# Kernel optimization log

Measured on AMD Instinct MI355X. Metric: run time of the kernel, lower is better.

Reference implementation:

```python
import jax, jax.numpy as jnp
import numpy as np

B, S, D = 32, 2048, 1024
E, K = 64, 8
N_TAGS = 128


def setup_inputs() -> dict:
    key = jax.random.key(0)
    k1, k2, k3, k4, k5, k6 = jax.random.split(key, 6)
    hidden_states = jax.random.normal(k1, (B, S, D), dtype=jnp.float32)
    subw_indices = jax.random.randint(k2, (B, E, K), 0, S, dtype=jnp.int32)
    subw_counts = jax.random.randint(k3, (B, E), 1, K + 1, dtype=jnp.int32)
    num_entities = jax.random.randint(k4, (B,), 1, E + 1, dtype=jnp.int32)
    fc_w = jax.random.normal(k5, (N_TAGS, D), dtype=jnp.float32) * (1.0 / np.sqrt(D))
    fc_b = jax.random.normal(k6, (N_TAGS,), dtype=jnp.float32) * 0.01
    return {
        "hidden_states": hidden_states,
        "subw_indices": subw_indices,
        "subw_counts": subw_counts,
        "num_entities": num_entities,
        "fc_w": fc_w,
        "fc_b": fc_b,
    }


def reference(hidden_states, subw_indices, subw_counts, num_entities, fc_w, fc_b):
    # Gather subword embeddings: [B, E, K, D]
    flat_idx = subw_indices.reshape(B, E * K)                      # [B, E*K]
    gathered = jnp.take_along_axis(
        hidden_states, flat_idx[:, :, None], axis=1
    ).reshape(B, E, K, D)
    # Mask padded subword slots and mean-pool per entity
    subw_mask = (jnp.arange(K)[None, None, :] < subw_counts[:, :, None])  # [B,E,K]
    subw_mask = subw_mask.astype(hidden_states.dtype)
    ent_emb = jnp.einsum("bekd,bek->bed", gathered, subw_mask)
    ent_emb = ent_emb / subw_counts[:, :, None].astype(hidden_states.dtype)
    # Zero-pad entities past num_entities (original pads with zero_emb)
    ent_mask = (jnp.arange(E)[None, :] < num_entities[:, None])    # [B,E]
    ent_emb = ent_emb * ent_mask[:, :, None].astype(hidden_states.dtype)
    # fc applied to all positions (padded rows yield the bias, as in original)
    logits = jnp.einsum("bed,td->bet", ent_emb, fc_w) + fc_b
    return logits
```

## Files before the change

kernel.cpp:

```cpp
#include <hip/hip_runtime.h>

#define BB 32
#define SS 2048
#define DD 1024
#define EE 64
#define KK 8
#define TT 128
#define MM (BB * EE)

#define MT 8
#define KC 128
#define ASTR 1032
#define WSTR 136

typedef __attribute__((ext_vector_type(8))) short short8;
typedef __attribute__((ext_vector_type(4))) float f32x4;

__device__ __forceinline__ unsigned short f2bf(float f) {
    union { float f; unsigned int u; } v; v.f = f;
    unsigned int u = v.u + 0x7FFFu + ((v.u >> 16) & 1u);
    return (unsigned short)(u >> 16);
}

__global__ __launch_bounds__(256) void te_fused_kernel(
    const float* __restrict__ hs,
    const int*   __restrict__ subw_idx,
    const int*   __restrict__ subw_cnt,
    const int*   __restrict__ num_ent,
    const float* __restrict__ fc_w,
    const float* __restrict__ fc_b,
    float* __restrict__ out)
{
    __shared__ unsigned short As[MT][ASTR];
    __shared__ unsigned short Ws[TT][WSTR];

    const int mt   = blockIdx.x;
    const int t    = threadIdx.x;
    const int wid  = t >> 6;
    const int lane = t & 63;

    {
        const int r  = t >> 5;
        const int c  = t & 31;
        const int be = mt * MT + r;
        const int b  = be >> 6;
        const int e  = be & 63;
        const int cnt = subw_cnt[be];
        const int ne  = num_ent[b];
        const float scale = (e < ne) ? (1.0f / (float)cnt) : 0.0f;
        const int* idxp = subw_idx + (size_t)be * KK;

        float4 acc4[8];
        #pragma unroll
        for (int j = 0; j < 8; ++j) acc4[j] = make_float4(0.f, 0.f, 0.f, 0.f);

        for (int k = 0; k < cnt; ++k) {
            const int s = idxp[k];
            const float4* row = (const float4*)(hs + ((size_t)b * SS + s) * DD);
            #pragma unroll
            for (int j = 0; j < 8; ++j) {
                float4 v = row[j * 32 + c];
                acc4[j].x += v.x; acc4[j].y += v.y;
                acc4[j].z += v.z; acc4[j].w += v.w;
            }
        }
        #pragma unroll
        for (int j = 0; j < 8; ++j) {
            ushort4 o;
            o.x = f2bf(acc4[j].x * scale); o.y = f2bf(acc4[j].y * scale);
            o.z = f2bf(acc4[j].z * scale); o.w = f2bf(acc4[j].w * scale);
            *(ushort4*)&As[r][(j * 32 + c) * 4] = o;
        }
    }

    const int nbase = wid * 32;
    const int lm  = lane & 15;
    const int lq  = (lane >> 4) * 8;
    const int lmA = lm & 7;

    f32x4 acc0 = {0.f,0.f,0.f,0.f}, acc1 = {0.f,0.f,0.f,0.f};

    const int n = t >> 1;
    const int h = (t & 1) * 64;

    for (int kc = 0; kc < DD / KC; ++kc) {
        __syncthreads();
        {
            const float4* wrow = (const float4*)(fc_w + (size_t)n * DD + kc * KC + h);
            #pragma unroll
            for (int j = 0; j < 16; ++j) {
                float4 v = wrow[j];
                ushort4 o;
                o.x = f2bf(v.x); o.y = f2bf(v.y);
                o.z = f2bf(v.z); o.w = f2bf(v.w);
                *(ushort4*)&Ws[n][h + j * 4] = o;
            }
        }
        __syncthreads();

        #pragma unroll
        for (int kstep = 0; kstep < KC / 32; ++kstep) {
            const int ko = kstep * 32 + lq;
            short8 a  = *(const short8*)&As[lmA][kc * KC + ko];
            short8 b0 = *(const short8*)&Ws[nbase +  0 + lm][ko];
            short8 b1 = *(const short8*)&Ws[nbase + 16 + lm][ko];
            acc0 = __builtin_amdgcn_mfma_f32_16x16x32_bf16(a, b0, acc0, 0, 0, 0);
            acc1 = __builtin_amdgcn_mfma_f32_16x16x32_bf16(a, b1, acc1, 0, 0, 0);
        }
    }

    if (lane < 32) {
        const int mrow = mt * MT + (lane >> 4) * 4;
        const int c0 = nbase + lm;
        const float b0v = fc_b[c0];
        const float b1v = fc_b[c0 + 16];
        #pragma unroll
        for (int r = 0; r < 4; ++r) {
            float* o = out + (size_t)(mrow + r) * TT + c0;
            o[0]  = acc0[r] + b0v;
            o[16] = acc1[r] + b1v;
        }
    }
}

extern "C" void kernel_launch(void* const* d_in, const int* in_sizes, int n_in,
                              void* d_out, int out_size, void* d_ws, size_t ws_size,
                              hipStream_t stream) {
    const float* hs       = (const float*)d_in[0];
    const int*   subw_idx = (const int*)  d_in[1];
    const int*   subw_cnt = (const int*)  d_in[2];
    const int*   num_ent  = (const int*)  d_in[3];
    const float* fc_w     = (const float*)d_in[4];
    const float* fc_b     = (const float*)d_in[5];
    float*       out      = (float*)d_out;

    te_fused_kernel<<<MM / MT, 256, 0, stream>>>(
        hs, subw_idx, subw_cnt, num_ent, fc_w, fc_b, out);
}
```

Measured before the change: 327.5 us.

## Split fused pool+GEMM into separate pooling and bf16 GEMM kernels

Replaces the single fused kernel with two launches. The first pools the gathered subword rows (one block per entity), writes bf16 entity embeddings to workspace, and converts fc_w to bf16 once. The second is an MFMA GEMM over 16-row tiles that reads the pre-converted bf16 data. This removes the per-block redundant fc_w fp32 reads and conversions (the weight matrix was reconverted by all 256 blocks) and the wasted half of each 16-row MFMA tile. The cost is an extra launch plus a workspace round-trip for the pooled embeddings.

```diff
diff --git a/kernel.cpp b/kernel.cpp
--- a/kernel.cpp
+++ b/kernel.cpp
@@ -8,8 +8,8 @@
 #define TT 128
 #define MM (BB * EE)
 
-#define MT 8
-#define KC 128
+#define GMT 16
+#define KC  128
 #define ASTR 1032
 #define WSTR 136
 
@@ -22,16 +22,54 @@
     return (unsigned short)(u >> 16);
 }
 
-__global__ __launch_bounds__(256) void te_fused_kernel(
+__global__ __launch_bounds__(256) void pool_kernel(
     const float* __restrict__ hs,
     const int*   __restrict__ subw_idx,
     const int*   __restrict__ subw_cnt,
     const int*   __restrict__ num_ent,
     const float* __restrict__ fc_w,
+    unsigned short* __restrict__ entb,
+    unsigned short* __restrict__ wb)
+{
+    const int be = blockIdx.x;
+    const int b  = be >> 6;
+    const int e  = be & 63;
+    const int t  = threadIdx.x;
+
+    const int cnt = subw_cnt[be];
+    const int ne  = num_ent[b];
+    const float scale = (e < ne) ? (1.0f / (float)cnt) : 0.0f;
+
+    const int* idxp = subw_idx + (size_t)be * KK;
+
+    float4 acc = make_float4(0.f, 0.f, 0.f, 0.f);
+    #pragma unroll
+    for (int k = 0; k < KK; ++k) {
+        if (k < cnt) {
+            const int s = idxp[k];
+            const float4* row = (const float4*)(hs + ((size_t)b * SS + s) * DD);
+            float4 v = row[t];
+            acc.x += v.x; acc.y += v.y; acc.z += v.z; acc.w += v.w;
+        }
+    }
+    ushort4 o;
+    o.x = f2bf(acc.x * scale); o.y = f2bf(acc.y * scale);
+    o.z = f2bf(acc.z * scale); o.w = f2bf(acc.w * scale);
+    *(ushort4*)(entb + (size_t)be * DD + 4 * t) = o;
+
+    if (t < 64) {
+        const int j = be * 64 + t;
+        wb[j] = f2bf(fc_w[j]);
+    }
+}
+
+__global__ __launch_bounds__(256) void gemm_kernel(
+    const unsigned short* __restrict__ entb,
+    const unsigned short* __restrict__ wb,
     const float* __restrict__ fc_b,
     float* __restrict__ out)
 {
-    __shared__ unsigned short As[MT][ASTR];
+    __shared__ unsigned short As[GMT][ASTR];
     __shared__ unsigned short Ws[TT][WSTR];
 
     const int mt   = blockIdx.x;
@@ -39,69 +77,37 @@
     const int wid  = t >> 6;
     const int lane = t & 63;
 
-    {
-        const int r  = t >> 5;
-        const int c  = t & 31;
-        const int be = mt * MT + r;
-        const int b  = be >> 6;
-        const int e  = be & 63;
-        const int cnt = subw_cnt[be];
-        const int ne  = num_ent[b];
-        const float scale = (e < ne) ? (1.0f / (float)cnt) : 0.0f;
-        const int* idxp = subw_idx + (size_t)be * KK;
-
-        float4 acc4[8];
-        #pragma unroll
-        for (int j = 0; j < 8; ++j) acc4[j] = make_float4(0.f, 0.f, 0.f, 0.f);
-
-        for (int k = 0; k < cnt; ++k) {
-            const int s = idxp[k];
-            const float4* row = (const float4*)(hs + ((size_t)b * SS + s) * DD);
-            #pragma unroll
-            for (int j = 0; j < 8; ++j) {
-                float4 v = row[j * 32 + c];
-                acc4[j].x += v.x; acc4[j].y += v.y;
-                acc4[j].z += v.z; acc4[j].w += v.w;
-            }
-        }
-        #pragma unroll
-        for (int j = 0; j < 8; ++j) {
-            ushort4 o;
-            o.x = f2bf(acc4[j].x * scale); o.y = f2bf(acc4[j].y * scale);
-            o.z = f2bf(acc4[j].z * scale); o.w = f2bf(acc4[j].w * scale);
-            *(ushort4*)&As[r][(j * 32 + c) * 4] = o;
-        }
+    #pragma unroll
+    for (int p = 0; p < 8; ++p) {
+        const int i   = p * 256 + t;
+        const int row = i >> 7;
+        const int c   = i & 127;
+        *(float4*)&As[row][c * 8] =
+            *(const float4*)(entb + (size_t)(mt * GMT + row) * DD + c * 8);
     }
 
     const int nbase = wid * 32;
-    const int lm  = lane & 15;
-    const int lq  = (lane >> 4) * 8;
-    const int lmA = lm & 7;
+    const int lm = lane & 15;
+    const int lq = (lane >> 4) * 8;
 
     f32x4 acc0 = {0.f,0.f,0.f,0.f}, acc1 = {0.f,0.f,0.f,0.f};
 
-    const int n = t >> 1;
-    const int h = (t & 1) * 64;
-
     for (int kc = 0; kc < DD / KC; ++kc) {
         __syncthreads();
-        {
-            const float4* wrow = (const float4*)(fc_w + (size_t)n * DD + kc * KC + h);
-            #pragma unroll
-            for (int j = 0; j < 16; ++j) {
-                float4 v = wrow[j];
-                ushort4 o;
-                o.x = f2bf(v.x); o.y = f2bf(v.y);
-                o.z = f2bf(v.z); o.w = f2bf(v.w);
-                *(ushort4*)&Ws[n][h + j * 4] = o;
-            }
+        #pragma unroll
+        for (int p = 0; p < 8; ++p) {
+            const int i   = p * 256 + t;
+            const int row = i >> 4;
+            const int c   = i & 15;
+            *(float4*)&Ws[row][c * 8] =
+                *(const float4*)(wb + (size_t)row * DD + kc * KC + c * 8);
         }
         __syncthreads();
 
         #pragma unroll
         for (int kstep = 0; kstep < KC / 32; ++kstep) {
             const int ko = kstep * 32 + lq;
-            short8 a  = *(const short8*)&As[lmA][kc * KC + ko];
+            short8 a  = *(const short8*)&As[lm][kc * KC + ko];
             short8 b0 = *(const short8*)&Ws[nbase +  0 + lm][ko];
             short8 b1 = *(const short8*)&Ws[nbase + 16 + lm][ko];
             acc0 = __builtin_amdgcn_mfma_f32_16x16x32_bf16(a, b0, acc0, 0, 0, 0);
@@ -109,17 +115,15 @@
         }
     }
 
-    if (lane < 32) {
-        const int mrow = mt * MT + (lane >> 4) * 4;
-        const int c0 = nbase + lm;
-        const float b0v = fc_b[c0];
-        const float b1v = fc_b[c0 + 16];
-        #pragma unroll
-        for (int r = 0; r < 4; ++r) {
-            float* o = out + (size_t)(mrow + r) * TT + c0;
-            o[0]  = acc0[r] + b0v;
-            o[16] = acc1[r] + b1v;
-        }
+    const int mrow = mt * GMT + (lane >> 4) * 4;
+    const int c0   = nbase + lm;
+    const float b0v = fc_b[c0];
+    const float b1v = fc_b[c0 + 16];
+    #pragma unroll
+    for (int r = 0; r < 4; ++r) {
+        float* o = out + (size_t)(mrow + r) * TT + c0;
+        o[0]  = acc0[r] + b0v;
+        o[16] = acc1[r] + b1v;
     }
 }
 
@@ -134,6 +138,10 @@
     const float* fc_b     = (const float*)d_in[5];
     float*       out      = (float*)d_out;
 
-    te_fused_kernel<<<MM / MT, 256, 0, stream>>>(
-        hs, subw_idx, subw_cnt, num_ent, fc_w, fc_b, out);
+    unsigned short* entb = (unsigned short*)d_ws;
+    unsigned short* wb   = (unsigned short*)((char*)d_ws + (size_t)MM * DD * 2);
+
+    pool_kernel<<<MM, 256, 0, stream>>>(hs, subw_idx, subw_cnt, num_ent,
+                                        fc_w, entb, wb);
+    gemm_kernel<<<MM / GMT, 256, 0, stream>>>(entb, wb, fc_b, out);
 }
```

New measurement: 319.9 us. 1.02x faster.
